# Kernel optimization log

Measured on AMD Instinct MI355X. Metric: run time of the kernel, lower is better.

The kernel has to match this reference:

```python
import jax, jax.numpy as jnp
import numpy as np

EPS = 1e-6
SIGMA_C = 2.0
PAD = 0
VOCAB = 100
D_EMB = 384


def setup_inputs() -> dict:
    key = jax.random.key(0)
    k1, k2, k3 = jax.random.split(key, 3)
    B, L = 32, 1025  # L odd so durs[:,1::2] and durs[:,2::2] align
    text = jax.random.randint(k1, (B, L), 0, VOCAB)
    durs = jax.random.randint(k2, (B, L), 0, 4)
    emb_table = jax.random.normal(k3, (VOCAB, D_EMB), dtype=jnp.float32)
    return {"text": text, "durs": durs, "emb_table": emb_table, "total_time": 2048}


def reference(text, durs, emb_table, total_time):
    # --- merge blank/token pairs (as in GaussianEmbedding.forward) ---
    text_m = jnp.concatenate([text[:, :1], text[:, 1::2]], axis=1)              # [B,N]
    durs_m = jnp.concatenate([durs[:, :1], durs[:, 1::2] + durs[:, 2::2]], axis=1)  # [B,N]
    embed = emb_table[text_m]                                                    # [B,N,E]

    # --- Gaussian length regulation ---
    d = durs_m.astype(jnp.float32)
    cum = jnp.cumsum(d, axis=-1)                 # [B,N] end times
    c = cum - 0.5 * d                            # [B,N] token centers
    sig = d / SIGMA_C + EPS                      # [B,N]
    t = jnp.arange(total_time, dtype=jnp.float32) + 0.5  # [T] frame midpoints

    # Normal pdf weights [B,T,N]
    z = (t[None, :, None] - c[:, None, :]) / sig[:, None, :]
    w = jnp.exp(-0.5 * z * z) / (sig[:, None, :] * jnp.sqrt(2.0 * jnp.pi))
    # zero weight for pad tokens, normalize over tokens
    w = jnp.where((text_m == PAD)[:, None, :], 0.0, w)
    w = w / (w.sum(-1, keepdims=True) + EPS)
    # zero frames beyond each sample's total duration
    valid = t[None, :] < cum[:, -1:]             # [B,T]
    w = jnp.where(valid[..., None], w, 0.0)

    return jnp.einsum('btn,bne->bte', w, embed)  # [B,T,E]
```

## Files before the change

kernel.cpp:

```cpp
#include <hip/hip_runtime.h>
#include <hip/hip_bf16.h>

#define BATCH 32
#define LSEQ 1025
#define TT 2048
#define NTOK 513
#define EMB 384
#define FT 32
#define NTILE (TT / FT)
#define WMAX 88
#define INV_SQRT_2PI 0.3989422804014327f

__global__ __launch_bounds__(256) void prep_kernel(
    const int* __restrict__ text, const int* __restrict__ durs,
    float2* __restrict__ kept, int2* __restrict__ tile_win,
    float* __restrict__ totals) {
  const int b = blockIdx.x;
  const int tid = threadIdx.x;
  const int lane = tid & 63;
  const int wv = tid >> 6;

  __shared__ float s_cc[NTOK];
  __shared__ float s_wd[4], s_wf[4];

  const int* tb = text + b * LSEQ;
  const int* db = durs + b * LSEQ;

  float d[3], fl[3];
  int tk[3];
  const int nbase = 3 * tid;
#pragma unroll
  for (int j = 0; j < 3; ++j) {
    const int n = nbase + j;
    int dm = 0, t = 0;
    if (n < NTOK) {
      if (n == 0) { dm = db[0]; t = tb[0]; }
      else { dm = db[2 * n - 1] + db[2 * n]; t = tb[2 * n - 1]; }
    }
    d[j] = (float)dm;
    tk[j] = t;
    fl[j] = (dm >= 1 && t != 0) ? 1.0f : 0.0f;
  }
  const float ld1 = d[0] + d[1], ld2 = ld1 + d[2];
  const float lf1 = fl[0] + fl[1], lf2 = lf1 + fl[2];

  float sd = ld2, sf = lf2;
#pragma unroll
  for (int off = 1; off < 64; off <<= 1) {
    const float od = __shfl_up(sd, off);
    const float of = __shfl_up(sf, off);
    if (lane >= off) { sd += od; sf += of; }
  }
  if (lane == 63) { s_wd[wv] = sd; s_wf[wv] = sf; }
  __syncthreads();

  float wod = 0.f, wof = 0.f;
#pragma unroll
  for (int k = 0; k < 4; ++k) {
    if (k < wv) { wod += s_wd[k]; wof += s_wf[k]; }
  }
  const float exd = wod + sd - ld2;
  const float exf = wof + sf - lf2;

  const float cum0 = exd + d[0], cum1 = exd + ld1, cum2 = exd + ld2;
  const float fin0 = exf + fl[0], fin1 = exf + lf1, fin2 = exf + lf2;
  const float cums[3] = {cum0, cum1, cum2};
  const float fins[3] = {fin0, fin1, fin2};

#pragma unroll
  for (int j = 0; j < 3; ++j) {
    const int n = nbase + j;
    if (n < NTOK && fl[j] > 0.f) {
      const int pos = (int)fins[j] - 1;
      const float c = cums[j] - 0.5f * d[j];
      const int packed = ((int)d[j] << 17) | (tk[j] * EMB);
      kept[b * NTOK + pos] = make_float2(c, __int_as_float(packed));
      s_cc[pos] = c;
    }
  }
  const float total = s_wd[0] + s_wd[1] + s_wd[2] + s_wd[3];
  const int M = (int)(s_wf[0] + s_wf[1] + s_wf[2] + s_wf[3]);
  if (tid == 0) totals[b] = total;
  __syncthreads();

  if (tid < NTILE) {
    const int t0 = tid * FT;
    const float loB = (float)t0 - 23.6f;
    const float hiB = (float)t0 + 55.6f;
    int l = 0, r = M;
    while (l < r) { const int m = (l + r) >> 1; if (s_cc[m] < loB) l = m + 1; else r = m; }
    const int lo = l;
    r = M;
    while (l < r) { const int m = (l + r) >> 1; if (s_cc[m] <= hiB) l = m + 1; else r = m; }
    int wn = l - lo;
    if (wn > WMAX) wn = WMAX;
    tile_win[b * NTILE + tid] = make_int2(lo, wn);
  }
}

__device__ inline void fma4(float4& a, const float w, const float4 v) {
  a.x += w * v.x; a.y += w * v.y; a.z += w * v.z; a.w += w * v.w;
}

__global__ __launch_bounds__(256) void frames_kernel(
    const float2* __restrict__ kept, const int2* __restrict__ tile_win,
    const float* __restrict__ totals, const float* __restrict__ emb,
    float* __restrict__ out) {
  const int tile = blockIdx.x;
  const int t0 = tile * FT;
  const int b = blockIdx.y;
  const int tid = threadIdx.x;

  __shared__ float4 s_tk[WMAX];
  __shared__ float s_reach[WMAX];
  __shared__ float s_w[WMAX * FT];
  __shared__ float s_factor[FT];

  const float total = totals[b];
  const int2 wininfo = tile_win[b * NTILE + tile];
  const int lo = wininfo.x;
  const int win = wininfo.y;
  const float2* kb = kept + b * NTOK;

  for (int i = tid; i < win; i += 256) {
    const float2 kv = kb[lo + i];
    const int packed = __float_as_int(kv.y);
    const int dI = packed >> 17;
    const float df = (float)dI;
    const float inv_sig = 1.0f / (0.5f * df + 1e-6f);
    s_tk[i] = make_float4(kv.x, inv_sig, INV_SQRT_2PI * inv_sig,
                          __int_as_float(packed & 0x1FFFF));
    s_reach[i] = 4.0f * df + 1e-4f;
  }
  __syncthreads();

  const float t0f = (float)t0 + 0.5f;
  const int pairs = win << 5;
  for (int idx = tid; idx < pairs; idx += 256) {
    const int n = idx >> 5, f = idx & (FT - 1);
    const float4 tk = s_tk[n];
    const float z = (t0f + (float)f - tk.x) * tk.y;
    s_w[idx] = tk.z * __expf(-0.5f * z * z);
  }
  __syncthreads();

  if (tid < FT) {
    float s = 0.f;
    for (int n = 0; n < win; ++n) s += s_w[(n << 5) + tid];
    const float tf = t0f + (float)tid;
    s_factor[tid] = (tf < total) ? 1.0f / (s + 1e-6f) : 0.0f;
  }
  __syncthreads();

  const int g = tid >> 5;
  const int c = (tid & 31) * 12;
  float4 acc[4][3];
#pragma unroll
  for (int j = 0; j < 4; ++j) {
#pragma unroll
    for (int k = 0; k < 3; ++k) acc[j][k] = make_float4(0.f, 0.f, 0.f, 0.f);
  }

  const float fLo = t0f + (float)(4 * g);
  const float fHi = fLo + 3.0f;
  for (int n = 0; n < win; ++n) {
    const float4 tk = s_tk[n];
    const float rc = s_reach[n];
    if (tk.x + rc < fLo || tk.x - rc > fHi) continue;
    const int off = __float_as_int(tk.w);
    const float4 w4 = *(const float4*)(s_w + (n << 5) + 4 * g);
    const float4 v0 = *(const float4*)(emb + off + c);
    const float4 v1 = *(const float4*)(emb + off + c + 4);
    const float4 v2 = *(const float4*)(emb + off + c + 8);
    const float wv_[4] = {w4.x, w4.y, w4.z, w4.w};
#pragma unroll
    for (int j = 0; j < 4; ++j) {
      const float w = wv_[j];
      fma4(acc[j][0], w, v0);
      fma4(acc[j][1], w, v1);
      fma4(acc[j][2], w, v2);
    }
  }

  float* op = out + ((size_t)b * TT + t0 + 4 * g) * EMB + c;
#pragma unroll
  for (int j = 0; j < 4; ++j) {
    const float fac = s_factor[4 * g + j];
    float* row = op + (size_t)j * EMB;
    float4 r0, r1, r2;
    r0.x = acc[j][0].x * fac; r0.y = acc[j][0].y * fac;
    r0.z = acc[j][0].z * fac; r0.w = acc[j][0].w * fac;
    r1.x = acc[j][1].x * fac; r1.y = acc[j][1].y * fac;
    r1.z = acc[j][1].z * fac; r1.w = acc[j][1].w * fac;
    r2.x = acc[j][2].x * fac; r2.y = acc[j][2].y * fac;
    r2.z = acc[j][2].z * fac; r2.w = acc[j][2].w * fac;
    *(float4*)(row) = r0;
    *(float4*)(row + 4) = r1;
    *(float4*)(row + 8) = r2;
  }
}

extern "C" void kernel_launch(void* const* d_in, const int* in_sizes, int n_in,
                              void* d_out, int out_size, void* d_ws,
                              size_t ws_size, hipStream_t stream) {
  const int* text = (const int*)d_in[0];
  const int* durs = (const int*)d_in[1];
  const float* emb = (const float*)d_in[2];
  float* out = (float*)d_out;

  float2* kept = (float2*)d_ws;
  int2* tile_win = (int2*)(kept + BATCH * NTOK);
  float* totals = (float*)(tile_win + BATCH * NTILE);

  prep_kernel<<<BATCH, 256, 0, stream>>>(text, durs, kept, tile_win, totals);
  frames_kernel<<<dim3(NTILE, BATCH), 256, 0, stream>>>(kept, tile_win, totals,
                                                        emb, out);
}
```

Baseline: 131.4 us.

## Retile frames accumulation to 16 frames x 4 columns per thread with nontemporal stores

The frames kernel now runs 192 threads per block. Each thread owns 4 embedding columns across 16 frames, where before it owned 12 columns across 4 frames. Each token row then needs one float4 global load per thread instead of three, and the output goes out through nontemporal stores. The trade-offs are a coarser per-thread token skip window (16 frames), which does more wasted FMAs on zero weights, and a 16-float4 accumulator that raises register pressure.

```diff
diff --git a/kernel.cpp b/kernel.cpp
--- a/kernel.cpp
+++ b/kernel.cpp
@@ -10,6 +10,8 @@
 #define NTILE (TT / FT)
 #define WMAX 88
 #define INV_SQRT_2PI 0.3989422804014327f
+
+typedef float floatx4 __attribute__((ext_vector_type(4)));
 
 __global__ __launch_bounds__(256) void prep_kernel(
     const int* __restrict__ text, const int* __restrict__ durs,
@@ -62,10 +64,8 @@
   const float exd = wod + sd - ld2;
   const float exf = wof + sf - lf2;
 
-  const float cum0 = exd + d[0], cum1 = exd + ld1, cum2 = exd + ld2;
-  const float fin0 = exf + fl[0], fin1 = exf + lf1, fin2 = exf + lf2;
-  const float cums[3] = {cum0, cum1, cum2};
-  const float fins[3] = {fin0, fin1, fin2};
+  const float cums[3] = {exd + d[0], exd + ld1, exd + ld2};
+  const float fins[3] = {exf + fl[0], exf + lf1, exf + lf2};
 
 #pragma unroll
   for (int j = 0; j < 3; ++j) {
@@ -98,11 +98,7 @@
   }
 }
 
-__device__ inline void fma4(float4& a, const float w, const float4 v) {
-  a.x += w * v.x; a.y += w * v.y; a.z += w * v.z; a.w += w * v.w;
-}
-
-__global__ __launch_bounds__(256) void frames_kernel(
+__global__ __launch_bounds__(192) void frames_kernel(
     const float2* __restrict__ kept, const int2* __restrict__ tile_win,
     const float* __restrict__ totals, const float* __restrict__ emb,
     float* __restrict__ out) {
@@ -122,7 +118,7 @@
   const int win = wininfo.y;
   const float2* kb = kept + b * NTOK;
 
-  for (int i = tid; i < win; i += 256) {
+  for (int i = tid; i < win; i += 192) {
     const float2 kv = kb[lo + i];
     const int packed = __float_as_int(kv.y);
     const int dI = packed >> 17;
@@ -136,7 +132,7 @@
 
   const float t0f = (float)t0 + 0.5f;
   const int pairs = win << 5;
-  for (int idx = tid; idx < pairs; idx += 256) {
+  for (int idx = tid; idx < pairs; idx += 192) {
     const int n = idx >> 5, f = idx & (FT - 1);
     const float4 tk = s_tk[n];
     const float z = (t0f + (float)f - tk.x) * tk.y;
@@ -152,51 +148,44 @@
   }
   __syncthreads();
 
-  const int g = tid >> 5;
-  const int c = (tid & 31) * 12;
-  float4 acc[4][3];
-#pragma unroll
-  for (int j = 0; j < 4; ++j) {
-#pragma unroll
-    for (int k = 0; k < 3; ++k) acc[j][k] = make_float4(0.f, 0.f, 0.f, 0.f);
-  }
-
-  const float fLo = t0f + (float)(4 * g);
-  const float fHi = fLo + 3.0f;
+  const int fh = tid / 96;
+  const int cg = (tid % 96) * 4;
+  const int fbase = fh * 16;
+  float4 acc[16];
+#pragma unroll
+  for (int k = 0; k < 16; ++k) acc[k] = make_float4(0.f, 0.f, 0.f, 0.f);
+
+  const float fLo = t0f + (float)fbase;
+  const float fHi = fLo + 15.0f;
   for (int n = 0; n < win; ++n) {
     const float4 tk = s_tk[n];
     const float rc = s_reach[n];
     if (tk.x + rc < fLo || tk.x - rc > fHi) continue;
     const int off = __float_as_int(tk.w);
-    const float4 w4 = *(const float4*)(s_w + (n << 5) + 4 * g);
-    const float4 v0 = *(const float4*)(emb + off + c);
-    const float4 v1 = *(const float4*)(emb + off + c + 4);
-    const float4 v2 = *(const float4*)(emb + off + c + 8);
-    const float wv_[4] = {w4.x, w4.y, w4.z, w4.w};
-#pragma unroll
-    for (int j = 0; j < 4; ++j) {
-      const float w = wv_[j];
-      fma4(acc[j][0], w, v0);
-      fma4(acc[j][1], w, v1);
-      fma4(acc[j][2], w, v2);
+    const float4 v = *(const float4*)(emb + off + cg);
+    const float4* wp = (const float4*)(s_w + (n << 5) + fbase);
+#pragma unroll
+    for (int q = 0; q < 4; ++q) {
+      const float4 w4 = wp[q];
+      float4& a0 = acc[4 * q + 0];
+      a0.x += w4.x * v.x; a0.y += w4.x * v.y; a0.z += w4.x * v.z; a0.w += w4.x * v.w;
+      float4& a1 = acc[4 * q + 1];
+      a1.x += w4.y * v.x; a1.y += w4.y * v.y; a1.z += w4.y * v.z; a1.w += w4.y * v.w;
+      float4& a2 = acc[4 * q + 2];
+      a2.x += w4.z * v.x; a2.y += w4.z * v.y; a2.z += w4.z * v.z; a2.w += w4.z * v.w;
+      float4& a3 = acc[4 * q + 3];
+      a3.x += w4.w * v.x; a3.y += w4.w * v.y; a3.z += w4.w * v.z; a3.w += w4.w * v.w;
     }
   }
 
-  float* op = out + ((size_t)b * TT + t0 + 4 * g) * EMB + c;
-#pragma unroll
-  for (int j = 0; j < 4; ++j) {
-    const float fac = s_factor[4 * g + j];
-    float* row = op + (size_t)j * EMB;
-    float4 r0, r1, r2;
-    r0.x = acc[j][0].x * fac; r0.y = acc[j][0].y * fac;
-    r0.z = acc[j][0].z * fac; r0.w = acc[j][0].w * fac;
-    r1.x = acc[j][1].x * fac; r1.y = acc[j][1].y * fac;
-    r1.z = acc[j][1].z * fac; r1.w = acc[j][1].w * fac;
-    r2.x = acc[j][2].x * fac; r2.y = acc[j][2].y * fac;
-    r2.z = acc[j][2].z * fac; r2.w = acc[j][2].w * fac;
-    *(float4*)(row) = r0;
-    *(float4*)(row + 4) = r1;
-    *(float4*)(row + 8) = r2;
+  const size_t obase = ((size_t)b * TT + t0 + fbase) * EMB + cg;
+#pragma unroll
+  for (int k = 0; k < 16; ++k) {
+    const float fac = s_factor[fbase + k];
+    floatx4 r;
+    r.x = acc[k].x * fac; r.y = acc[k].y * fac;
+    r.z = acc[k].z * fac; r.w = acc[k].w * fac;
+    __builtin_nontemporal_store(r, (floatx4*)(out + obase + (size_t)k * EMB));
   }
 }
 
@@ -213,6 +202,6 @@
   float* totals = (float*)(tile_win + BATCH * NTILE);
 
   prep_kernel<<<BATCH, 256, 0, stream>>>(text, durs, kept, tile_win, totals);
-  frames_kernel<<<dim3(NTILE, BATCH), 256, 0, stream>>>(kept, tile_win, totals,
+  frames_kernel<<<dim3(NTILE, BATCH), 192, 0, stream>>>(kept, tile_win, totals,
                                                         emb, out);
 }
```

Result: faster. 125.1 us (-4.8%).
